# Performance work log

Measured on AMD Instinct MI355X. Metric: run time of the kernel, lower is better.

Reference implementation:

```python
import jax, jax.numpy as jnp
import numpy as np

N = 50000
E = 800000
NEG_SLOPE = 0.2  # PyG GATConv default


def _glorot(key, shape, scale=0.1):
    return jax.random.normal(key, shape, dtype=jnp.float32) * scale


def setup_inputs() -> dict:
    key = jax.random.key(0)
    ks = jax.random.split(key, 16)
    X = jax.random.normal(ks[0], (N, 128), dtype=jnp.float32)
    edge_index = jax.random.randint(ks[1], (2, E), 0, N, dtype=jnp.int64)
    edge_weight = jax.random.uniform(ks[2], (E,), dtype=jnp.float32)
    # GATConv layer params: W [in,out], att_src/att_dst [out], bias [out]
    W1, as1, ad1, b1 = _glorot(ks[3], (128, 128)), _glorot(ks[4], (128,)), _glorot(ks[5], (128,)), jnp.zeros((128,), jnp.float32)
    W2, as2, ad2, b2 = _glorot(ks[6], (128, 64)), _glorot(ks[7], (64,)), _glorot(ks[8], (64,)), jnp.zeros((64,), jnp.float32)
    W3, as3, ad3, b3 = _glorot(ks[9], (64, 32)), _glorot(ks[10], (32,)), _glorot(ks[11], (32,)), jnp.zeros((32,), jnp.float32)
    Wl, bl = _glorot(ks[12], (32, 1)), jnp.zeros((1,), jnp.float32)
    return {"X": X, "edge_index": edge_index, "edge_weight": edge_weight,
            "W1": W1, "as1": as1, "ad1": ad1, "b1": b1,
            "W2": W2, "as2": as2, "ad2": ad2, "b2": b2,
            "W3": W3, "as3": as3, "ad3": ad3, "b3": b3,
            "Wl": Wl, "bl": bl}


def gat_layer(x, src, dst, W, a_src, a_dst, b):
    # x: [N, in] -> h: [N, out]
    h = x @ W
    # per-node attention logits, gathered per edge
    alpha = jax.nn.leaky_relu((h * a_src).sum(-1)[src] + (h * a_dst).sum(-1)[dst], NEG_SLOPE)  # [E']
    # segment-softmax over incoming edges of each dst node
    amax = jax.ops.segment_max(alpha, dst, num_segments=N)
    ex = jnp.exp(alpha - amax[dst])
    denom = jax.ops.segment_sum(ex, dst, num_segments=N)
    w = ex / (denom[dst] + 1e-16)
    # scatter-add weighted messages
    out = jax.ops.segment_sum(h[src] * w[:, None], dst, num_segments=N)
    return out + b


def reference(X, edge_index, edge_weight, W1, as1, ad1, b1, W2, as2, ad2, b2, W3, as3, ad3, b3, Wl, bl):
    # GATConv add_self_loops=True: append self loops (static shape)
    loops = jnp.arange(N, dtype=edge_index.dtype)
    src = jnp.concatenate([edge_index[0], loops])
    dst = jnp.concatenate([edge_index[1], loops])
    # edge_weight is ignored by PyG GATConv when edge_dim is None (faithful)
    x = jax.nn.elu(gat_layer(X, src, dst, W1, as1, ad1, b1))
    x = jax.nn.elu(gat_layer(x, src, dst, W2, as2, ad2, b2))
    x = jax.nn.elu(gat_layer(x, src, dst, W3, as3, ad3, b3))
    x = x @ Wl + bl
    return jax.nn.sigmoid(x)[:, 0]
```

## Files before the change

kernel.cpp:

```cpp
#include <hip/hip_runtime.h>
#include <hip/hip_bf16.h>

typedef __attribute__((ext_vector_type(8))) short bf16x8;
typedef __attribute__((ext_vector_type(4))) float f32x4;

constexpr int NBMAX = 128;
constexpr int EPB   = 2048;
constexpr int CAP   = 12288;


__device__ __forceinline__ float bf2f(unsigned short u) {
    union { unsigned int i; float f; } c; c.i = ((unsigned int)u) << 16; return c.f;
}
__device__ __forceinline__ unsigned short f2bf(float f) {
    union { unsigned int i; float f; } c; c.f = f;
    unsigned int i = c.i;
    unsigned int r = (i + 0x7FFFu + ((i >> 16) & 1u)) >> 16;
    return (unsigned short)r;
}


__device__ __forceinline__ void pack_one(const float* __restrict__ W, int K, int OUT, int idx,
                                         unsigned short* __restrict__ hi, unsigned short* __restrict__ lo) {
    int KS = K >> 5;
    int lane = idx & 63;
    int rest = idx >> 6;
    int ks = rest % KS, ct = rest / KS;
    int m = lane & 15, kg = lane >> 4;
    size_t base = (size_t)idx * 8;
#pragma unroll
    for (int j = 0; j < 8; ++j) {
        float w = W[(size_t)(ks * 32 + kg * 8 + j) * OUT + ct * 16 + m];
        unsigned short h = f2bf(w);
        hi[base + j] = h;
        lo[base + j] = f2bf(w - bf2f(h));
    }
}

__global__ void pack_init(const float* __restrict__ W1, unsigned short* hi1, unsigned short* lo1,
                          const float* __restrict__ W2, unsigned short* hi2, unsigned short* lo2,
                          const float* __restrict__ W3, unsigned short* hi3, unsigned short* lo3,
                          int* __restrict__ cursor, int nb) {
    if (blockIdx.x < 13) {
        int idx = blockIdx.x * 256 + threadIdx.x;
        if (idx < 2048)               pack_one(W1, 128, 128, idx, hi1, lo1);
        else if (idx < 2048 + 1024)   pack_one(W2, 128,  64, idx - 2048, hi2, lo2);
        else if (idx < 2048 + 1280)   pack_one(W3,  64,  32, idx - 3072, hi3, lo3);
    } else {
        int t = threadIdx.x;
        if (t < nb) cursor[t] = t * CAP;
    }
}


__global__ __launch_bounds__(256) void bin_passA(const int* __restrict__ ei, int E, int N, int nb,
                                                 int* __restrict__ cursor,
                                                 unsigned int* __restrict__ stageG) {
    __shared__ int bcnt[NBMAX], bofs[NBMAX], gbase[NBMAX], bfill[NBMAX];
    __shared__ unsigned int stage[EPB];
    const int t = threadIdx.x;
    const int Et = E + N;
    const int e0 = blockIdx.x * EPB;
    const int ecnt = min(EPB, Et - e0);
    if (t < nb) { bcnt[t] = 0; bfill[t] = 0; }
    __syncthreads();
    unsigned int pk[8];
#pragma unroll
    for (int k = 0; k < 8; ++k) {
        int e = e0 + t + k * 256;
        pk[k] = 0xFFFFFFFFu;
        if (e < Et) {
            int s, d;
            if (e < E) { s = ei[e]; d = ei[E + e]; } else { s = d = e - E; }
            pk[k] = ((unsigned int)d << 16) | (unsigned int)s;
            atomicAdd(&bcnt[d >> 9], 1);
        }
    }
    __syncthreads();
    if (t == 0) {
        int run = 0;
        for (int i = 0; i < nb; ++i) { bofs[i] = run; run += bcnt[i]; }
    }
    __syncthreads();
    if (t < nb && bcnt[t] > 0) gbase[t] = atomicAdd(&cursor[t], bcnt[t]);
    __syncthreads();
#pragma unroll
    for (int k = 0; k < 8; ++k) {
        if (pk[k] != 0xFFFFFFFFu) {
            int b = pk[k] >> 25;
            int pos = bofs[b] + atomicAdd(&bfill[b], 1);
            stage[pos] = pk[k];
        }
    }
    __syncthreads();
    for (int i = t; i < ecnt; i += 256) {
        unsigned int p = stage[i];
        int b = p >> 25;
        stageG[(size_t)gbase[b] + (i - bofs[b])] = p;
    }
}


template <int K, int OUT>
__device__ __forceinline__ void gemm_body(const float* __restrict__ X,
                                          const unsigned short* __restrict__ Whi,
                                          const unsigned short* __restrict__ Wlo,
                                          const float* __restrict__ avs,
                                          const float* __restrict__ avd,
                                          unsigned short* __restrict__ Hb,
                                          float* __restrict__ asrc,
                                          float* __restrict__ adst, int N, int waveIdx) {
    constexpr int CT = OUT / 16, KS = K / 32;
    const int lane = threadIdx.x & 63;
    const int row0 = waveIdx << 4;
    if (row0 >= N) return;
    const int m = lane & 15, kg = lane >> 4;
    f32x4 acc[CT];
#pragma unroll
    for (int c = 0; c < CT; ++c) acc[c] = (f32x4){0.f, 0.f, 0.f, 0.f};
    const float* xrow = X + (size_t)(row0 + m) * K + kg * 8;
    const bf16x8* whf = (const bf16x8*)Whi;
    const bf16x8* wlf = (const bf16x8*)Wlo;
#pragma unroll
    for (int ks = 0; ks < KS; ++ks) {
        float4 x0 = *reinterpret_cast<const float4*>(xrow + ks * 32);
        float4 x1 = *reinterpret_cast<const float4*>(xrow + ks * 32 + 4);
        float xv[8] = {x0.x, x0.y, x0.z, x0.w, x1.x, x1.y, x1.z, x1.w};
        bf16x8 xhi, xlo;
#pragma unroll
        for (int j = 0; j < 8; ++j) {
            unsigned short h = f2bf(xv[j]);
            xhi[j] = (short)h;
            xlo[j] = (short)f2bf(xv[j] - bf2f(h));
        }
#pragma unroll
        for (int c = 0; c < CT; ++c) {
            bf16x8 wh = whf[(c * KS + ks) * 64 + lane];
            bf16x8 wl = wlf[(c * KS + ks) * 64 + lane];
            acc[c] = __builtin_amdgcn_mfma_f32_16x16x32_bf16(wh, xhi, acc[c], 0, 0, 0);
            acc[c] = __builtin_amdgcn_mfma_f32_16x16x32_bf16(wl, xhi, acc[c], 0, 0, 0);
            acc[c] = __builtin_amdgcn_mfma_f32_16x16x32_bf16(wh, xlo, acc[c], 0, 0, 0);
        }
    }
    float s = 0.f, d = 0.f;
    const size_t hbase = (size_t)(row0 + m) * OUT;
#pragma unroll
    for (int c = 0; c < CT; ++c) {
        const int col = c * 16 + kg * 4;
        float4 av = *reinterpret_cast<const float4*>(avs + col);
        float4 dv = *reinterpret_cast<const float4*>(avd + col);
        s += acc[c][0] * av.x + acc[c][1] * av.y + acc[c][2] * av.z + acc[c][3] * av.w;
        d += acc[c][0] * dv.x + acc[c][1] * dv.y + acc[c][2] * dv.z + acc[c][3] * dv.w;
        uint2 u;
        u.x = (unsigned int)f2bf(acc[c][0]) | ((unsigned int)f2bf(acc[c][1]) << 16);
        u.y = (unsigned int)f2bf(acc[c][2]) | ((unsigned int)f2bf(acc[c][3]) << 16);
        *reinterpret_cast<uint2*>(Hb + hbase + col) = u;
    }
    s += __shfl_xor(s, 16); s += __shfl_xor(s, 32);
    d += __shfl_xor(d, 16); d += __shfl_xor(d, 32);
    if (lane < 16) { asrc[row0 + lane] = s; adst[row0 + lane] = d; }
}

template <int K, int OUT>
__global__ __launch_bounds__(256) void gemm_attn_mfma(const float* __restrict__ X,
                                                      const unsigned short* __restrict__ Whi,
                                                      const unsigned short* __restrict__ Wlo,
                                                      const float* __restrict__ avs,
                                                      const float* __restrict__ avd,
                                                      unsigned short* __restrict__ Hb,
                                                      float* __restrict__ asrc,
                                                      float* __restrict__ adst, int N) {
    gemm_body<K, OUT>(X, Whi, Wlo, avs, avd, Hb, asrc, adst, N,
                      blockIdx.x * 4 + (threadIdx.x >> 6));
}


__global__ __launch_bounds__(512) void passB_gemm1(int nb, const int* __restrict__ cursor,
                                                   const unsigned int* __restrict__ stageG,
                                                   int* __restrict__ rowptr,
                                                   unsigned short* __restrict__ csrc,
                                                   int Et, int N,
                                                   const float* __restrict__ X,
                                                   const unsigned short* __restrict__ Whi,
                                                   const unsigned short* __restrict__ Wlo,
                                                   const float* __restrict__ avs,
                                                   const float* __restrict__ avd,
                                                   unsigned short* __restrict__ Hb,
                                                   float* __restrict__ asrc,
                                                   float* __restrict__ adst) {
    if ((int)blockIdx.x >= nb) {
        gemm_body<128, 128>(X, Whi, Wlo, avs, avd, Hb, asrc, adst, N,
                            (blockIdx.x - nb) * 8 + (threadIdx.x >> 6));
        return;
    }
    __shared__ int cnt[512], sofs[512], cnt2[512];
    __shared__ int tot[NBMAX];
    __shared__ unsigned short cs[CAP];
    __shared__ int rowbase_s, total_s;
    const int b = blockIdx.x, t = threadIdx.x;
    if (t < nb) tot[t] = cursor[t] - t * CAP;
    cnt[t] = 0; cnt2[t] = 0;
    __syncthreads();
    if (t == 0) {
        int run = 0;
        for (int i = 0; i < b; ++i) run += tot[i];
        rowbase_s = run; total_s = tot[b];
    }
    __syncthreads();
    const int tB = total_s, rb = rowbase_s;
    const unsigned int* sg = stageG + (size_t)b * CAP;
    for (int i = t; i < tB; i += 512) atomicAdd(&cnt[(sg[i] >> 16) & 511], 1);
    __syncthreads();
    int v = cnt[t];
    sofs[t] = v;
    __syncthreads();
    for (int off = 1; off < 512; off <<= 1) {
        int x = (t >= off) ? sofs[t - off] : 0;
        __syncthreads();
        sofs[t] += x;
        __syncthreads();
    }
    const int excl = sofs[t] - v;
    const int d = (b << 9) + t;
    if (d < N) rowptr[d] = rb + excl;
    if (b == nb - 1 && t == 0) rowptr[N] = Et;
    __syncthreads();
    sofs[t] = excl;
    __syncthreads();
    for (int i = t; i < tB; i += 512) {
        unsigned int p = sg[i];
        int ld = (p >> 16) & 511;
        int pos = sofs[ld] + atomicAdd(&cnt2[ld], 1);
        cs[pos] = (unsigned short)(p & 0xFFFFu);
    }
    __syncthreads();
    for (int i = t; i < tB; i += 512) csrc[rb + i] = cs[i];
}


template <int OUT, bool FINAL>
__global__ __launch_bounds__(256) void gat_aggregate(const unsigned short* __restrict__ Hb,
                                                     const float* __restrict__ asrc,
                                                     const float* __restrict__ adst,
                                                     const int* __restrict__ rowptr,
                                                     const unsigned short* __restrict__ csrc,
                                                     const float* __restrict__ bias,
                                                     float* __restrict__ Xout,
                                                     const float* __restrict__ Wl,
                                                     const float* __restrict__ bl,
                                                     float* __restrict__ fout, int N) {
    constexpr int SUBW = OUT / 4;
    constexpr int NPW = 64 / SUBW;
    __shared__ float2 pair[4][64];
    const int wslot = threadIdx.x >> 6;
    const int lane = threadIdx.x & 63;
    const int sub = lane / SUBW;
    const int sl  = lane % SUBW;
    const int wid = (blockIdx.x * blockDim.x + threadIdx.x) >> 6;
    const int node = wid * NPW + sub;
    if (node >= N) return;
    const int beg = rowptr[node], end = rowptr[node + 1];
    const float ad = adst[node];
    float m = -1e30f;
    for (int j = beg + sl; j < end; j += SUBW) {
        float a = asrc[csrc[j]] + ad;
        m = fmaxf(m, a > 0.f ? a : 0.2f * a);
    }
#pragma unroll
    for (int off = SUBW / 2; off; off >>= 1) m = fmaxf(m, __shfl_xor(m, off));
    float dsum = 0.f;
    for (int j = beg + sl; j < end; j += SUBW) {
        float a = asrc[csrc[j]] + ad;
        a = a > 0.f ? a : 0.2f * a;
        dsum += __expf(a - m);
    }
#pragma unroll
    for (int off = SUBW / 2; off; off >>= 1) dsum += __shfl_xor(dsum, off);
    const float inv = 1.0f / (dsum + 1e-16f);
    const int k4 = sl * 4;
    float a0 = 0.f, a1 = 0.f, a2 = 0.f, a3 = 0.f;
    for (int cbeg = beg; cbeg < end; cbeg += SUBW) {
        const int cnt = min(SUBW, end - cbeg);
        if (sl < cnt) {
            int s = csrc[cbeg + sl];
            float a = asrc[s] + ad;
            a = a > 0.f ? a : 0.2f * a;
            pair[wslot][lane] = make_float2(__expf(a - m) * inv, __int_as_float(s));
        }
#pragma unroll 4
        for (int u = 0; u < cnt; ++u) {
            float2 p = pair[wslot][sub * SUBW + u];
            int s = __float_as_int(p.y);
            uint2 hu = *reinterpret_cast<const uint2*>(Hb + (size_t)s * OUT + k4);
            a0 += __uint_as_float(hu.x << 16) * p.x;
            a1 += __uint_as_float(hu.x & 0xffff0000u) * p.x;
            a2 += __uint_as_float(hu.y << 16) * p.x;
            a3 += __uint_as_float(hu.y & 0xffff0000u) * p.x;
        }
    }
    float4 bi = *reinterpret_cast<const float4*>(bias + k4);
    float v0 = a0 + bi.x, v1 = a1 + bi.y, v2 = a2 + bi.z, v3 = a3 + bi.w;
    v0 = v0 > 0.f ? v0 : expm1f(v0);
    v1 = v1 > 0.f ? v1 : expm1f(v1);
    v2 = v2 > 0.f ? v2 : expm1f(v2);
    v3 = v3 > 0.f ? v3 : expm1f(v3);
    if (FINAL) {
        float4 wl = *reinterpret_cast<const float4*>(Wl + k4);
        float part = v0 * wl.x + v1 * wl.y + v2 * wl.z + v3 * wl.w;
#pragma unroll
        for (int off = SUBW / 2; off; off >>= 1) part += __shfl_xor(part, off);
        if (sl == 0) fout[node] = 1.f / (1.f + __expf(-(part + bl[0])));
    } else {
        *reinterpret_cast<float4*>(Xout + (size_t)node * OUT + k4) = make_float4(v0, v1, v2, v3);
    }
}


extern "C" void kernel_launch(void* const* d_in, const int* in_sizes, int n_in,
                              void* d_out, int out_size, void* d_ws, size_t ws_size,
                              hipStream_t stream) {
    const float* X   = (const float*)d_in[0];
    const int*   ei  = (const int*)d_in[1];
    const float* W1  = (const float*)d_in[3];
    const float* a1s = (const float*)d_in[4];
    const float* a1d = (const float*)d_in[5];
    const float* b1  = (const float*)d_in[6];
    const float* W2  = (const float*)d_in[7];
    const float* a2s = (const float*)d_in[8];
    const float* a2d = (const float*)d_in[9];
    const float* b2  = (const float*)d_in[10];
    const float* W3  = (const float*)d_in[11];
    const float* a3s = (const float*)d_in[12];
    const float* a3d = (const float*)d_in[13];
    const float* b3  = (const float*)d_in[14];
    const float* Wl  = (const float*)d_in[15];
    const float* bl  = (const float*)d_in[16];
    float* out = (float*)d_out;

    const int N  = in_sizes[0] / 128;
    const int E  = in_sizes[1] / 2;
    const int Et = E + N;
    const int nb = (N + 511) >> 9;
    (void)n_in; (void)out_size; (void)ws_size;

    char* w = (char*)d_ws;
    size_t o = 0;
    auto alloc = [&](size_t bytes) -> void* {
        void* p = w + o;
        o += (bytes + 255) & ~(size_t)255;
        return p;
    };
    unsigned short* csrc = (unsigned short*)alloc((size_t)Et * 2);
    int*   rowptr   = (int*)alloc((size_t)(N + 1) * 4);
    int*   cursor   = (int*)alloc(NBMAX * 4);
    unsigned int* stageG = (unsigned int*)alloc((size_t)nb * CAP * 4);
    float* asrc     = (float*)alloc((size_t)N * 4);
    float* adst     = (float*)alloc((size_t)N * 4);
    unsigned short* Hb = (unsigned short*)alloc((size_t)N * 128 * 2);
    float* XA       = (float*)alloc((size_t)N * 128 * 4);
    float* XB       = (float*)alloc((size_t)N * 64 * 4);
    unsigned short* whi1 = (unsigned short*)alloc(8 * 4 * 64 * 8 * 2);
    unsigned short* wlo1 = (unsigned short*)alloc(8 * 4 * 64 * 8 * 2);
    unsigned short* whi2 = (unsigned short*)alloc(4 * 4 * 64 * 8 * 2);
    unsigned short* wlo2 = (unsigned short*)alloc(4 * 4 * 64 * 8 * 2);
    unsigned short* whi3 = (unsigned short*)alloc(2 * 2 * 64 * 8 * 2);
    unsigned short* wlo3 = (unsigned short*)alloc(2 * 2 * 64 * 8 * 2);

    hipLaunchKernelGGL(pack_init, dim3(14), dim3(256), 0, stream,
                       W1, whi1, wlo1, W2, whi2, wlo2, W3, whi3, wlo3, cursor, nb);

    hipLaunchKernelGGL(bin_passA, dim3((Et + EPB - 1) / EPB), dim3(256), 0, stream,
                       ei, E, N, nb, cursor, stageG);

    const int gemmBlocks512 = (N + 127) / 128;
    hipLaunchKernelGGL(passB_gemm1, dim3(nb + gemmBlocks512), dim3(512), 0, stream,
                       nb, cursor, stageG, rowptr, csrc, Et, N,
                       X, whi1, wlo1, a1s, a1d, Hb, asrc, adst);

    hipLaunchKernelGGL((gat_aggregate<128, false>), dim3((N + 7) / 8), dim3(256), 0, stream,
                       Hb, asrc, adst, rowptr, csrc, b1, XA, nullptr, nullptr, nullptr, N);

    const int gemmBlocks = (N + 63) / 64;
    hipLaunchKernelGGL((gemm_attn_mfma<128, 64>), dim3(gemmBlocks), dim3(256), 0, stream,
                       XA, whi2, wlo2, a2s, a2d, Hb, asrc, adst, N);
    hipLaunchKernelGGL((gat_aggregate<64, false>), dim3((N + 15) / 16), dim3(256), 0, stream,
                       Hb, asrc, adst, rowptr, csrc, b2, XB, nullptr, nullptr, nullptr, N);

    hipLaunchKernelGGL((gemm_attn_mfma<64, 32>), dim3(gemmBlocks), dim3(256), 0, stream,
                       XB, whi3, wlo3, a3s, a3d, Hb, asrc, adst, N);
    hipLaunchKernelGGL((gat_aggregate<32, true>), dim3((N + 31) / 32), dim3(256), 0, stream,
                       Hb, asrc, adst, rowptr, csrc, b3, nullptr, Wl, bl, out, N);
}
```

Before: 153.8 us.

## Store intermediate activations in bf16 and fuse softmax into a single aggregation pass

Layers 1 and 2 now write their ELU outputs as bf16 rather than fp32, and a new bf16-input GEMM feeds the MFMA directly without converting X. The aggregation kernel drops its separate max and sum passes over each node's edges. It accumulates exp(alpha) unnormalized, sums the denominator alongside, and normalizes at the end. This halves intermediate traffic and removes two gathers of asrc per edge, but skipping the max subtraction risks exp overflow for large logits, and bf16 activations lose precision.

```diff
diff --git a/kernel.cpp b/kernel.cpp
--- a/kernel.cpp
+++ b/kernel.cpp
@@ -161,8 +161,9 @@
     if (lane < 16) { asrc[row0 + lane] = s; adst[row0 + lane] = d; }
 }
 
+
 template <int K, int OUT>
-__global__ __launch_bounds__(256) void gemm_attn_mfma(const float* __restrict__ X,
+__global__ __launch_bounds__(256) void gemm_attn_bf16(const unsigned short* __restrict__ Xb,
                                                       const unsigned short* __restrict__ Whi,
                                                       const unsigned short* __restrict__ Wlo,
                                                       const float* __restrict__ avs,
@@ -170,8 +171,45 @@
                                                       unsigned short* __restrict__ Hb,
                                                       float* __restrict__ asrc,
                                                       float* __restrict__ adst, int N) {
-    gemm_body<K, OUT>(X, Whi, Wlo, avs, avd, Hb, asrc, adst, N,
-                      blockIdx.x * 4 + (threadIdx.x >> 6));
+    constexpr int CT = OUT / 16, KS = K / 32;
+    const int lane = threadIdx.x & 63;
+    const int row0 = (blockIdx.x * 4 + (threadIdx.x >> 6)) << 4;
+    if (row0 >= N) return;
+    const int m = lane & 15, kg = lane >> 4;
+    f32x4 acc[CT];
+#pragma unroll
+    for (int c = 0; c < CT; ++c) acc[c] = (f32x4){0.f, 0.f, 0.f, 0.f};
+    const unsigned short* xrow = Xb + (size_t)(row0 + m) * K + kg * 8;
+    const bf16x8* whf = (const bf16x8*)Whi;
+    const bf16x8* wlf = (const bf16x8*)Wlo;
+#pragma unroll
+    for (int ks = 0; ks < KS; ++ks) {
+        bf16x8 x = *reinterpret_cast<const bf16x8*>(xrow + ks * 32);
+#pragma unroll
+        for (int c = 0; c < CT; ++c) {
+            bf16x8 wh = whf[(c * KS + ks) * 64 + lane];
+            bf16x8 wl = wlf[(c * KS + ks) * 64 + lane];
+            acc[c] = __builtin_amdgcn_mfma_f32_16x16x32_bf16(wh, x, acc[c], 0, 0, 0);
+            acc[c] = __builtin_amdgcn_mfma_f32_16x16x32_bf16(wl, x, acc[c], 0, 0, 0);
+        }
+    }
+    float s = 0.f, d = 0.f;
+    const size_t hbase = (size_t)(row0 + m) * OUT;
+#pragma unroll
+    for (int c = 0; c < CT; ++c) {
+        const int col = c * 16 + kg * 4;
+        float4 av = *reinterpret_cast<const float4*>(avs + col);
+        float4 dv = *reinterpret_cast<const float4*>(avd + col);
+        s += acc[c][0] * av.x + acc[c][1] * av.y + acc[c][2] * av.z + acc[c][3] * av.w;
+        d += acc[c][0] * dv.x + acc[c][1] * dv.y + acc[c][2] * dv.z + acc[c][3] * dv.w;
+        uint2 u;
+        u.x = (unsigned int)f2bf(acc[c][0]) | ((unsigned int)f2bf(acc[c][1]) << 16);
+        u.y = (unsigned int)f2bf(acc[c][2]) | ((unsigned int)f2bf(acc[c][3]) << 16);
+        *reinterpret_cast<uint2*>(Hb + hbase + col) = u;
+    }
+    s += __shfl_xor(s, 16); s += __shfl_xor(s, 32);
+    d += __shfl_xor(d, 16); d += __shfl_xor(d, 32);
+    if (lane < 16) { asrc[row0 + lane] = s; adst[row0 + lane] = d; }
 }
 
 
@@ -238,14 +276,14 @@
 }
 
 
-template <int OUT, bool FINAL>
+template <int OUT, int MODE>
 __global__ __launch_bounds__(256) void gat_aggregate(const unsigned short* __restrict__ Hb,
                                                      const float* __restrict__ asrc,
                                                      const float* __restrict__ adst,
                                                      const int* __restrict__ rowptr,
                                                      const unsigned short* __restrict__ csrc,
                                                      const float* __restrict__ bias,
-                                                     float* __restrict__ Xout,
+                                                     unsigned short* __restrict__ Xout,
                                                      const float* __restrict__ Wl,
                                                      const float* __restrict__ bl,
                                                      float* __restrict__ fout, int N) {
@@ -261,31 +299,18 @@
     if (node >= N) return;
     const int beg = rowptr[node], end = rowptr[node + 1];
     const float ad = adst[node];
-    float m = -1e30f;
-    for (int j = beg + sl; j < end; j += SUBW) {
-        float a = asrc[csrc[j]] + ad;
-        m = fmaxf(m, a > 0.f ? a : 0.2f * a);
-    }
-#pragma unroll
-    for (int off = SUBW / 2; off; off >>= 1) m = fmaxf(m, __shfl_xor(m, off));
-    float dsum = 0.f;
-    for (int j = beg + sl; j < end; j += SUBW) {
-        float a = asrc[csrc[j]] + ad;
-        a = a > 0.f ? a : 0.2f * a;
-        dsum += __expf(a - m);
-    }
-#pragma unroll
-    for (int off = SUBW / 2; off; off >>= 1) dsum += __shfl_xor(dsum, off);
-    const float inv = 1.0f / (dsum + 1e-16f);
     const int k4 = sl * 4;
     float a0 = 0.f, a1 = 0.f, a2 = 0.f, a3 = 0.f;
+    float dpart = 0.f;
     for (int cbeg = beg; cbeg < end; cbeg += SUBW) {
         const int cnt = min(SUBW, end - cbeg);
         if (sl < cnt) {
             int s = csrc[cbeg + sl];
             float a = asrc[s] + ad;
             a = a > 0.f ? a : 0.2f * a;
-            pair[wslot][lane] = make_float2(__expf(a - m) * inv, __int_as_float(s));
+            float u = __expf(a);
+            dpart += u;
+            pair[wslot][lane] = make_float2(u, __int_as_float(s));
         }
 #pragma unroll 4
         for (int u = 0; u < cnt; ++u) {
@@ -298,20 +323,27 @@
             a3 += __uint_as_float(hu.y & 0xffff0000u) * p.x;
         }
     }
+#pragma unroll
+    for (int off = SUBW / 2; off; off >>= 1) dpart += __shfl_xor(dpart, off);
+    const float inv = 1.0f / (dpart + 1e-16f);
     float4 bi = *reinterpret_cast<const float4*>(bias + k4);
-    float v0 = a0 + bi.x, v1 = a1 + bi.y, v2 = a2 + bi.z, v3 = a3 + bi.w;
+    float v0 = a0 * inv + bi.x, v1 = a1 * inv + bi.y;
+    float v2 = a2 * inv + bi.z, v3 = a3 * inv + bi.w;
     v0 = v0 > 0.f ? v0 : expm1f(v0);
     v1 = v1 > 0.f ? v1 : expm1f(v1);
     v2 = v2 > 0.f ? v2 : expm1f(v2);
     v3 = v3 > 0.f ? v3 : expm1f(v3);
-    if (FINAL) {
+    if (MODE == 1) {
         float4 wl = *reinterpret_cast<const float4*>(Wl + k4);
         float part = v0 * wl.x + v1 * wl.y + v2 * wl.z + v3 * wl.w;
 #pragma unroll
         for (int off = SUBW / 2; off; off >>= 1) part += __shfl_xor(part, off);
         if (sl == 0) fout[node] = 1.f / (1.f + __expf(-(part + bl[0])));
     } else {
-        *reinterpret_cast<float4*>(Xout + (size_t)node * OUT + k4) = make_float4(v0, v1, v2, v3);
+        uint2 u;
+        u.x = (unsigned int)f2bf(v0) | ((unsigned int)f2bf(v1) << 16);
+        u.y = (unsigned int)f2bf(v2) | ((unsigned int)f2bf(v3) << 16);
+        *reinterpret_cast<uint2*>(Xout + (size_t)node * OUT + k4) = u;
     }
 }
 
@@ -356,9 +388,9 @@
     unsigned int* stageG = (unsigned int*)alloc((size_t)nb * CAP * 4);
     float* asrc     = (float*)alloc((size_t)N * 4);
     float* adst     = (float*)alloc((size_t)N * 4);
-    unsigned short* Hb = (unsigned short*)alloc((size_t)N * 128 * 2);
-    float* XA       = (float*)alloc((size_t)N * 128 * 4);
-    float* XB       = (float*)alloc((size_t)N * 64 * 4);
+    unsigned short* Hb  = (unsigned short*)alloc((size_t)N * 128 * 2);
+    unsigned short* XAb = (unsigned short*)alloc((size_t)N * 128 * 2);
+    unsigned short* XBb = (unsigned short*)alloc((size_t)N * 64 * 2);
     unsigned short* whi1 = (unsigned short*)alloc(8 * 4 * 64 * 8 * 2);
     unsigned short* wlo1 = (unsigned short*)alloc(8 * 4 * 64 * 8 * 2);
     unsigned short* whi2 = (unsigned short*)alloc(4 * 4 * 64 * 8 * 2);
@@ -377,17 +409,17 @@
                        nb, cursor, stageG, rowptr, csrc, Et, N,
                        X, whi1, wlo1, a1s, a1d, Hb, asrc, adst);
 
-    hipLaunchKernelGGL((gat_aggregate<128, false>), dim3((N + 7) / 8), dim3(256), 0, stream,
-                       Hb, asrc, adst, rowptr, csrc, b1, XA, nullptr, nullptr, nullptr, N);
+    hipLaunchKernelGGL((gat_aggregate<128, 0>), dim3((N + 7) / 8), dim3(256), 0, stream,
+                       Hb, asrc, adst, rowptr, csrc, b1, XAb, nullptr, nullptr, nullptr, N);
 
     const int gemmBlocks = (N + 63) / 64;
-    hipLaunchKernelGGL((gemm_attn_mfma<128, 64>), dim3(gemmBlocks), dim3(256), 0, stream,
-                       XA, whi2, wlo2, a2s, a2d, Hb, asrc, adst, N);
-    hipLaunchKernelGGL((gat_aggregate<64, false>), dim3((N + 15) / 16), dim3(256), 0, stream,
-                       Hb, asrc, adst, rowptr, csrc, b2, XB, nullptr, nullptr, nullptr, N);
-
-    hipLaunchKernelGGL((gemm_attn_mfma<64, 32>), dim3(gemmBlocks), dim3(256), 0, stream,
-                       XB, whi3, wlo3, a3s, a3d, Hb, asrc, adst, N);
-    hipLaunchKernelGGL((gat_aggregate<32, true>), dim3((N + 31) / 32), dim3(256), 0, stream,
+    hipLaunchKernelGGL((gemm_attn_bf16<128, 64>), dim3(gemmBlocks), dim3(256), 0, stream,
+                       XAb, whi2, wlo2, a2s, a2d, Hb, asrc, adst, N);
+    hipLaunchKernelGGL((gat_aggregate<64, 0>), dim3((N + 15) / 16), dim3(256), 0, stream,
+                       Hb, asrc, adst, rowptr, csrc, b2, XBb, nullptr, nullptr, nullptr, N);
+
+    hipLaunchKernelGGL((gemm_attn_bf16<64, 32>), dim3(gemmBlocks), dim3(256), 0, stream,
+                       XBb, whi3, wlo3, a3s, a3d, Hb, asrc, adst, N);
+    hipLaunchKernelGGL((gat_aggregate<32, 1>), dim3((N + 31) / 32), dim3(256), 0, stream,
                        Hb, asrc, adst, rowptr, csrc, b3, nullptr, Wl, bl, out, N);
 }
```

Measured after the change: 133.0 us. 13.5% less time.
